# Kernel tuning notes

Measured on AMD Instinct MI355X. Metric: run time of the kernel, lower is better.

## Reference

```python
import jax, jax.numpy as jnp
import numpy as np

N_NODES = 100000


def gcn_conv(x, W, b, src, dst, n_nodes):
    """PyG-style GCNConv: add self-loops, symmetric D^-1/2 (A+I) D^-1/2 normalization,
    linear transform, scatter-add aggregation, bias."""
    h = x @ W  # [N, out]
    # add self-loops
    loop = jnp.arange(n_nodes, dtype=src.dtype)
    src_all = jnp.concatenate([src, loop])
    dst_all = jnp.concatenate([dst, loop])
    # degree (of A + I) counted at destination nodes
    deg = jax.ops.segment_sum(jnp.ones_like(dst_all, dtype=h.dtype), dst_all,
                              num_segments=n_nodes)
    dinv = jnp.where(deg > 0, jax.lax.rsqrt(deg), 0.0)  # [N]
    w = dinv[src_all] * dinv[dst_all]                   # per-edge norm
    msg = h[src_all] * w[:, None]                       # gather + scale
    out = jax.ops.segment_sum(msg, dst_all, num_segments=n_nodes)
    return out + b


def setup_inputs() -> dict:
    key = jax.random.key(0)
    k1, k2, k3, k4 = jax.random.split(key, 4)
    n, e = N_NODES, 1600000
    d_in, d_hid, d_out = 128, 128, 64
    x = jax.random.normal(k1, (n, d_in), dtype=jnp.float32)
    edge_index = jax.random.randint(k2, (2, e), 0, n, dtype=jnp.int64)
    W1 = jax.random.normal(k3, (d_in, d_hid), dtype=jnp.float32) / np.sqrt(d_in)
    b1 = jnp.zeros((d_hid,), dtype=jnp.float32)
    W2 = jax.random.normal(k4, (d_hid, d_out), dtype=jnp.float32) / np.sqrt(d_hid)
    b2 = jnp.zeros((d_out,), dtype=jnp.float32)
    return {"x": x, "edge_index": edge_index, "W1": W1, "b1": b1, "W2": W2, "b2": b2}


def reference(x, edge_index, W1, b1, W2, b2):
    src, dst = edge_index[0], edge_index[1]
    h = jax.nn.relu(gcn_conv(x, W1, b1, src, dst, N_NODES))
    return gcn_conv(h, W2, b2, src, dst, N_NODES)
```

## Files before the change

kernel.cpp:

```cpp
#include <hip/hip_runtime.h>
#include <hip/hip_fp16.h>


typedef _Float16 half8 __attribute__((ext_vector_type(8)));
typedef float f32x4 __attribute__((ext_vector_type(4)));

constexpr int BK_SHIFT = 7;
constexpr int BK_NODES = 1 << BK_SHIFT;
constexpr int NB_MAX   = 1024;
constexpr int SLAB     = 2560;
constexpr int P1_EPT   = 32;
constexpr int P1_EDGES = 256 * P1_EPT;

__global__ __launch_bounds__(256) void k_p1(const int* __restrict__ src,
                                            const int* __restrict__ dst, int E,
                                            int NB, int* __restrict__ bfill,
                                            unsigned* __restrict__ slab) {
  __shared__ unsigned stage[P1_EDGES];
  __shared__ unsigned short bidp[P1_EDGES];
  __shared__ int hist[NB_MAX];
  __shared__ int lbase[NB_MAX];
  __shared__ int goff[NB_MAX];
  __shared__ int part[256];

  const int t = threadIdx.x;
  const long base = (long)blockIdx.x * P1_EDGES;
  const int nval = (int)(((long)E - base < (long)P1_EDGES) ? (E - base) : P1_EDGES);

  for (int i = t; i < NB; i += 256) hist[i] = 0;
  __syncthreads();

  int eb[P1_EPT];
  unsigned ev[P1_EPT];
#pragma unroll
  for (int i = 0; i < P1_EPT; ++i) {
    long e = base + t + i * 256;
    int b = -1;
    unsigned v = 0;
    if (e < E) {
      int d = dst[e];
      int s = src[e];
      b = d >> BK_SHIFT;
      v = ((unsigned)(d & (BK_NODES - 1)) << 17) | (unsigned)s;
      atomicAdd(&hist[b], 1);
    }
    eb[i] = b;
    ev[i] = v;
  }
  __syncthreads();

  int lc[4];
  int lsum = 0;
#pragma unroll
  for (int j = 0; j < 4; ++j) {
    int b = t * 4 + j;
    lc[j] = (b < NB) ? hist[b] : 0;
    lsum += lc[j];
  }
  part[t] = lsum;
  __syncthreads();
  for (int o = 1; o < 256; o <<= 1) {
    int a = (t >= o) ? part[t - o] : 0;
    __syncthreads();
    part[t] += a;
    __syncthreads();
  }
  int run = part[t] - lsum;
#pragma unroll
  for (int j = 0; j < 4; ++j) {
    int b = t * 4 + j;
    if (b < NB) lbase[b] = run;
    run += lc[j];
  }
  __syncthreads();

  for (int b = t; b < NB; b += 256) {
    int len = hist[b];
    int g = len ? atomicAdd(&bfill[b], len) : 0;
    goff[b] = b * SLAB + g - lbase[b];
  }
  __syncthreads();

#pragma unroll
  for (int i = 0; i < P1_EPT; ++i) {
    if (eb[i] >= 0) {
      int p = atomicAdd(&lbase[eb[i]], 1);
      stage[p] = ev[i];
      bidp[p] = (unsigned short)eb[i];
    }
  }
  __syncthreads();

  for (int p = t; p < nval; p += 256) {
    int b = bidp[p];
    slab[goff[b] + p] = stage[p];
  }
}

__global__ __launch_bounds__(1024) void k_bscan(const int* __restrict__ bfill, int NB,
                                                int* __restrict__ bbase) {
  __shared__ int sm[1024];
  const int t = threadIdx.x;
  int v = (t < NB) ? bfill[t] : 0;
  sm[t] = v;
  __syncthreads();
  for (int o = 1; o < 1024; o <<= 1) {
    int a = (t >= o) ? sm[t - o] : 0;
    __syncthreads();
    sm[t] += a;
    __syncthreads();
  }
  if (t < NB) bbase[t] = sm[t] - v;
}

__global__ __launch_bounds__(256) void k_p2(const unsigned* __restrict__ slab,
                                            const int* __restrict__ bfill,
                                            const int* __restrict__ bbase, int N,
                                            int* __restrict__ deg,
                                            int* __restrict__ row_ptr,
                                            float* __restrict__ dinv,
                                            int* __restrict__ ssrc) {
  __shared__ int hist[BK_NODES];
  __shared__ int lb[BK_NODES];
  const int b = blockIdx.x;
  const int t = threadIdx.x;
  const int len = bfill[b];
  const int gbase = bbase[b];
  const unsigned* seg = slab + (size_t)b * SLAB;

  if (t < BK_NODES) hist[t] = 0;
  __syncthreads();
  for (int i = t; i < len; i += 256) atomicAdd(&hist[seg[i] >> 17], 1);
  __syncthreads();

  if (t < BK_NODES) lb[t] = hist[t];
  __syncthreads();
  for (int o = 1; o < BK_NODES; o <<= 1) {
    int a = 0;
    if (t < BK_NODES && t >= o) a = lb[t - o];
    __syncthreads();
    if (t < BK_NODES) lb[t] += a;
    __syncthreads();
  }

  int n = b * BK_NODES + t;
  if (t < BK_NODES && n < N) {
    int d = hist[t];
    deg[n] = d;
    row_ptr[n] = gbase + lb[t] - d;
    dinv[n] = rsqrtf((float)(d + 1));
  }
  __syncthreads();
  if (t < BK_NODES) lb[t] -= hist[t];
  __syncthreads();

  for (int i = t; i < len; i += 256) {
    unsigned v = seg[i];
    int l = v >> 17;
    int p = atomicAdd(&lb[l], 1);
    ssrc[gbase + p] = (int)(v & 0x1FFFF);
  }
}

__global__ __launch_bounds__(256) void k_prep(const float* __restrict__ W1,
                                              const float* __restrict__ W2,
                                              __half* __restrict__ Wt1,
                                              __half* __restrict__ Wt2) {
  int i = blockIdx.x * blockDim.x + threadIdx.x;
  if (i < 16384) {
    int k = i >> 7, n = i & 127;
    Wt1[n * 128 + k] = __float2half(W1[i]);
  } else if (i < 24576) {
    int j = i - 16384;
    int k = j >> 6, n = j & 63;
    Wt2[n * 128 + k] = __float2half(W2[j]);
  }
}

template <int NC, bool IN_HALF>
__global__ __launch_bounds__(256) void k_gemm(const void* __restrict__ Xv,
                                              const __half* __restrict__ Wt,
                                              const float* __restrict__ dinv,
                                              __half* __restrict__ H, int N) {
  constexpr int K = 128;
  constexpr int BM = 64;
  constexpr int LDK = K + 8;
  constexpr int NT = NC / 16;
  __shared__ _Float16 xs[BM * LDK];
  __shared__ _Float16 wl[NC * LDK];

  const int t = threadIdx.x;
  const int r0 = blockIdx.x * BM;

  if (IN_HALF) {
    const __half* X = (const __half*)Xv;
    for (int i = t; i < BM * (K / 8); i += 256) {
      int row = i >> 4, kc = i & 15;
      float4 raw = make_float4(0.f, 0.f, 0.f, 0.f);
      if (r0 + row < N)
        raw = *reinterpret_cast<const float4*>(X + (size_t)(r0 + row) * K + 8 * kc);
      *reinterpret_cast<float4*>(&xs[row * LDK + 8 * kc]) = raw;
    }
  } else {
    const float* X = (const float*)Xv;
    for (int i = t; i < BM * (K / 4); i += 256) {
      int row = i >> 5, kg = i & 31;
      float4 v = make_float4(0.f, 0.f, 0.f, 0.f);
      if (r0 + row < N)
        v = *reinterpret_cast<const float4*>(X + (size_t)(r0 + row) * K + 4 * kg);
      union { _Float16 h[4]; unsigned long long u; } pk;
      pk.h[0] = (_Float16)v.x; pk.h[1] = (_Float16)v.y;
      pk.h[2] = (_Float16)v.z; pk.h[3] = (_Float16)v.w;
      *reinterpret_cast<unsigned long long*>(&xs[row * LDK + 4 * kg]) = pk.u;
    }
  }
  for (int i = t; i < NC * (K / 8); i += 256) {
    int n = i >> 4, kc = i & 15;
    float4 raw = *reinterpret_cast<const float4*>(Wt + (size_t)n * K + 8 * kc);
    *reinterpret_cast<float4*>(&wl[n * LDK + 8 * kc]) = raw;
  }
  __syncthreads();

  const int w = t >> 6;
  const int lane = t & 63;
  const int lm = lane & 15;
  const int lg = lane >> 4;

  half8 a[4];
#pragma unroll
  for (int kt = 0; kt < 4; ++kt)
    a[kt] = *reinterpret_cast<const half8*>(&xs[(w * 16 + lm) * LDK + kt * 32 + lg * 8]);

  f32x4 acc[NT];
#pragma unroll
  for (int nt = 0; nt < NT; ++nt) acc[nt] = (f32x4){0.f, 0.f, 0.f, 0.f};

#pragma unroll
  for (int nt = 0; nt < NT; ++nt) {
#pragma unroll
    for (int kt = 0; kt < 4; ++kt) {
      half8 b = *reinterpret_cast<const half8*>(
          &wl[(nt * 16 + lm) * LDK + kt * 32 + lg * 8]);
      acc[nt] = __builtin_amdgcn_mfma_f32_16x16x32_f16(a[kt], b, acc[nt], 0, 0, 0);
    }
  }

  float dv[4];
#pragma unroll
  for (int r = 0; r < 4; ++r) {
    int row = r0 + w * 16 + lg * 4 + r;
    dv[r] = (row < N) ? dinv[row] : 0.f;
  }
#pragma unroll
  for (int nt = 0; nt < NT; ++nt) {
#pragma unroll
    for (int r = 0; r < 4; ++r) {
      int row = r0 + w * 16 + lg * 4 + r;
      if (row < N)
        H[(size_t)row * NC + nt * 16 + lm] = __float2half(acc[nt][r] * dv[r]);
    }
  }
}

__global__ __launch_bounds__(256) void k_agg128(const __half* __restrict__ H,
                                                const int* __restrict__ rp,
                                                const int* __restrict__ dg,
                                                const int* __restrict__ ssrc,
                                                const float* __restrict__ dinv,
                                                const float* __restrict__ bias,
                                                __half* __restrict__ out, int N) {
  const int wave = threadIdx.x >> 6;
  const int lane = threadIdx.x & 63;
  const int n = blockIdx.x * 4 + wave;
  if (n >= N) return;

  const int eh = lane >> 4;
  const int cl = lane & 15;
  const int e0 = rp[n];
  const int e1 = e0 + dg[n];
  const float dv = dinv[n];

  float acc[8] = {0.f, 0.f, 0.f, 0.f, 0.f, 0.f, 0.f, 0.f};
  auto gat = [&](int s) {
    half8 v = *reinterpret_cast<const half8*>(H + (size_t)s * 128 + 8 * cl);
#pragma unroll
    for (int j = 0; j < 8; ++j) acc[j] += (float)v[j];
  };
  if (eh == 0) gat(n);
  int e = e0;
  for (; e + 8 <= e1; e += 8) {
    int sA = ssrc[e + eh];
    int sB = ssrc[e + 4 + eh];
    gat(sA);
    gat(sB);
  }
  if (e + 4 <= e1) { gat(ssrc[e + eh]); e += 4; }
  if (e + eh < e1) gat(ssrc[e + eh]);

#pragma unroll
  for (int j = 0; j < 8; ++j) {
    acc[j] += __shfl_xor(acc[j], 16);
    acc[j] += __shfl_xor(acc[j], 32);
  }
  if (eh == 0) {
    float4 b0 = *reinterpret_cast<const float4*>(bias + 8 * cl);
    float4 b1 = *reinterpret_cast<const float4*>(bias + 8 * cl + 4);
    float o[8];
    o[0] = acc[0] * dv + b0.x; o[1] = acc[1] * dv + b0.y;
    o[2] = acc[2] * dv + b0.z; o[3] = acc[3] * dv + b0.w;
    o[4] = acc[4] * dv + b1.x; o[5] = acc[5] * dv + b1.y;
    o[6] = acc[6] * dv + b1.z; o[7] = acc[7] * dv + b1.w;
    half8 ph;
#pragma unroll
    for (int j = 0; j < 8; ++j) ph[j] = (_Float16)fmaxf(o[j], 0.f);
    *reinterpret_cast<half8*>(out + (size_t)n * 128 + 8 * cl) = ph;
  }
}

__global__ __launch_bounds__(256) void k_agg64(const __half* __restrict__ H,
                                               const int* __restrict__ rp,
                                               const int* __restrict__ dg,
                                               const int* __restrict__ ssrc,
                                               const float* __restrict__ dinv,
                                               const float* __restrict__ bias,
                                               float* __restrict__ out, int N) {
  const int wave = threadIdx.x >> 6;
  const int lane = threadIdx.x & 63;
  const int n = blockIdx.x * 4 + wave;
  if (n >= N) return;

  const int eh = lane >> 3;
  const int cl = lane & 7;
  const int e0 = rp[n];
  const int e1 = e0 + dg[n];
  const float dv = dinv[n];

  float acc[8] = {0.f, 0.f, 0.f, 0.f, 0.f, 0.f, 0.f, 0.f};
  auto gat = [&](int s) {
    half8 v = *reinterpret_cast<const half8*>(H + (size_t)s * 64 + 8 * cl);
#pragma unroll
    for (int j = 0; j < 8; ++j) acc[j] += (float)v[j];
  };
  if (eh == 0) gat(n);
  int e = e0;
  for (; e + 16 <= e1; e += 16) {
    int sA = ssrc[e + eh];
    int sB = ssrc[e + 8 + eh];
    gat(sA);
    gat(sB);
  }
  if (e + 8 <= e1) { gat(ssrc[e + eh]); e += 8; }
  if (e + eh < e1) gat(ssrc[e + eh]);

#pragma unroll
  for (int j = 0; j < 8; ++j) {
    acc[j] += __shfl_xor(acc[j], 8);
    acc[j] += __shfl_xor(acc[j], 16);
    acc[j] += __shfl_xor(acc[j], 32);
  }
  if (eh == 0) {
    float4 b0 = *reinterpret_cast<const float4*>(bias + 8 * cl);
    float4 b1 = *reinterpret_cast<const float4*>(bias + 8 * cl + 4);
    f32x4 o0, o1;
    o0[0] = acc[0] * dv + b0.x; o0[1] = acc[1] * dv + b0.y;
    o0[2] = acc[2] * dv + b0.z; o0[3] = acc[3] * dv + b0.w;
    o1[0] = acc[4] * dv + b1.x; o1[1] = acc[5] * dv + b1.y;
    o1[2] = acc[6] * dv + b1.z; o1[3] = acc[7] * dv + b1.w;
    float* op = out + (size_t)n * 64 + 8 * cl;
    __builtin_nontemporal_store(o0, reinterpret_cast<f32x4*>(op));
    __builtin_nontemporal_store(o1, reinterpret_cast<f32x4*>(op + 4));
  }
}

extern "C" void kernel_launch(void* const* d_in, const int* in_sizes, int n_in,
                              void* d_out, int out_size, void* d_ws, size_t ws_size,
                              hipStream_t stream) {
  const float* x = (const float*)d_in[0];
  const int* ei = (const int*)d_in[1];
  const float* W1 = (const float*)d_in[2];
  const float* b1 = (const float*)d_in[3];
  const float* W2 = (const float*)d_in[4];
  const float* b2 = (const float*)d_in[5];

  const int K = 128;
  const int N = in_sizes[0] / K;
  const int E = in_sizes[1] / 2;
  const int NB = (N + BK_NODES - 1) >> BK_SHIFT;
  if (NB > NB_MAX) return;

  const int* src = ei;
  const int* dst = ei + E;

  size_t off = 0;
  auto carve = [&](size_t bytes) {
    size_t o = off;
    off += (bytes + 255) & ~(size_t)255;
    return o;
  };
  char* ws = (char*)d_ws;
  int*      deg     = (int*)(ws + carve((size_t)N * 4));
  int*      row_ptr = (int*)(ws + carve((size_t)N * 4));
  float*    dinv    = (float*)(ws + carve((size_t)N * 4));
  int*      bfill   = (int*)(ws + carve((size_t)NB * 4));
  int*      bbase   = (int*)(ws + carve((size_t)NB * 4));
  __half*   wt1     = (__half*)(ws + carve(16384 * 2));
  __half*   wt2     = (__half*)(ws + carve(8192 * 2));
  unsigned* slab    = (unsigned*)(ws + carve((size_t)NB * SLAB * 4));
  int*      ssrc    = (int*)(ws + carve((size_t)E * 4));
  __half*   h1      = (__half*)(ws + carve((size_t)N * K * 2));
  __half*   out1    = (__half*)(ws + carve((size_t)N * K * 2));
  if (off > ws_size) return;

  __half* h2 = h1;
  float* out2 = (float*)d_out;

  (void)hipMemsetAsync(bfill, 0, (size_t)NB * 4, stream);
  k_prep<<<96, 256, 0, stream>>>(W1, W2, wt1, wt2);
  const int nwg1 = (E + P1_EDGES - 1) / P1_EDGES;
  k_p1<<<nwg1, 256, 0, stream>>>(src, dst, E, NB, bfill, slab);
  k_bscan<<<1, 1024, 0, stream>>>(bfill, NB, bbase);
  k_p2<<<NB, 256, 0, stream>>>(slab, bfill, bbase, N, deg, row_ptr, dinv, ssrc);

  k_gemm<128, false><<<(N + 63) / 64, 256, 0, stream>>>(x, wt1, dinv, h1, N);
  k_agg128<<<(N + 3) / 4, 256, 0, stream>>>(h1, row_ptr, deg, ssrc, dinv, b1,
                                            out1, N);
  k_gemm<64, true><<<(N + 63) / 64, 256, 0, stream>>>(out1, wt2, dinv, h2, N);
  k_agg64<<<(N + 3) / 4, 256, 0, stream>>>(h2, row_ptr, deg, ssrc, dinv, b2,
                                           out2, N);
  (void)n_in; (void)out_size;
}
```

Measured before the change: 201.1 us.

## Split layer-1 features into two 64-column slabs for cache-friendly aggregation

The first GEMM now writes its fp16 output as two contiguous column slabs of 64 features each, instead of interleaved 128-wide rows. The layer-1 aggregation launches twice as many blocks, one per slice, and each wave gathers 128-byte rows from a single slab with 8 edges in flight per step. The aim is to halve the working set each gather pass touches, so the random neighbor reads hit L2/MALL more often. The cost is reading the index stream and running the edge loop twice.

```diff
diff --git a/kernel.cpp b/kernel.cpp
--- a/kernel.cpp
+++ b/kernel.cpp
@@ -177,7 +177,7 @@
   }
 }
 
-template <int NC, bool IN_HALF>
+template <int NC, bool IN_HALF, bool OUT_SLAB>
 __global__ __launch_bounds__(256) void k_gemm(const void* __restrict__ Xv,
                                               const __half* __restrict__ Wt,
                                               const float* __restrict__ dinv,
@@ -256,55 +256,68 @@
 #pragma unroll
     for (int r = 0; r < 4; ++r) {
       int row = r0 + w * 16 + lg * 4 + r;
-      if (row < N)
-        H[(size_t)row * NC + nt * 16 + lm] = __float2half(acc[nt][r] * dv[r]);
-    }
-  }
-}
-
-__global__ __launch_bounds__(256) void k_agg128(const __half* __restrict__ H,
-                                                const int* __restrict__ rp,
-                                                const int* __restrict__ dg,
-                                                const int* __restrict__ ssrc,
-                                                const float* __restrict__ dinv,
-                                                const float* __restrict__ bias,
-                                                __half* __restrict__ out, int N) {
+      if (row < N) {
+        _Float16 val = (_Float16)(acc[nt][r] * dv[r]);
+        if (OUT_SLAB) {
+          int sl = nt >> 2;
+          int cc = (nt & 3) * 16 + lm;
+          *(_Float16*)(H + (size_t)sl * N * 64 + (size_t)row * 64 + cc) = val;
+        } else {
+          *(_Float16*)(H + (size_t)row * NC + nt * 16 + lm) = val;
+        }
+      }
+    }
+  }
+}
+
+__global__ __launch_bounds__(256) void k_agg128s(const __half* __restrict__ Hs,
+                                                 const int* __restrict__ rp,
+                                                 const int* __restrict__ dg,
+                                                 const int* __restrict__ ssrc,
+                                                 const float* __restrict__ dinv,
+                                                 const float* __restrict__ bias,
+                                                 __half* __restrict__ out, int N) {
+  const int slice = blockIdx.x & 1;
+  const int g = blockIdx.x >> 1;
   const int wave = threadIdx.x >> 6;
   const int lane = threadIdx.x & 63;
-  const int n = blockIdx.x * 4 + wave;
+  const int n = g * 4 + wave;
   if (n >= N) return;
 
-  const int eh = lane >> 4;
-  const int cl = lane & 15;
+  const int eh = lane >> 3;
+  const int cl = lane & 7;
+  const __half* __restrict__ sp = Hs + (size_t)slice * N * 64;
   const int e0 = rp[n];
   const int e1 = e0 + dg[n];
   const float dv = dinv[n];
 
   float acc[8] = {0.f, 0.f, 0.f, 0.f, 0.f, 0.f, 0.f, 0.f};
   auto gat = [&](int s) {
-    half8 v = *reinterpret_cast<const half8*>(H + (size_t)s * 128 + 8 * cl);
+    half8 v = *reinterpret_cast<const half8*>(sp + (size_t)s * 64 + 8 * cl);
 #pragma unroll
     for (int j = 0; j < 8; ++j) acc[j] += (float)v[j];
   };
   if (eh == 0) gat(n);
   int e = e0;
-  for (; e + 8 <= e1; e += 8) {
+  for (; e + 16 <= e1; e += 16) {
     int sA = ssrc[e + eh];
-    int sB = ssrc[e + 4 + eh];
+    int sB = ssrc[e + 8 + eh];
     gat(sA);
     gat(sB);
   }
-  if (e + 4 <= e1) { gat(ssrc[e + eh]); e += 4; }
+  if (e + 8 <= e1) { gat(ssrc[e + eh]); e += 8; }
   if (e + eh < e1) gat(ssrc[e + eh]);
 
 #pragma unroll
   for (int j = 0; j < 8; ++j) {
+    acc[j] += __shfl_xor(acc[j], 8);
     acc[j] += __shfl_xor(acc[j], 16);
     acc[j] += __shfl_xor(acc[j], 32);
   }
   if (eh == 0) {
-    float4 b0 = *reinterpret_cast<const float4*>(bias + 8 * cl);
-    float4 b1 = *reinterpret_cast<const float4*>(bias + 8 * cl + 4);
+    const float* bp = bias + slice * 64 + 8 * cl;
+    float4 b0 = *reinterpret_cast<const float4*>(bp);
+    float4 b1 = *reinterpret_cast<const float4*>(bp + 4);
     float o[8];
     o[0] = acc[0] * dv + b0.x; o[1] = acc[1] * dv + b0.y;
     o[2] = acc[2] * dv + b0.z; o[3] = acc[3] * dv + b0.w;
@@ -313,7 +326,7 @@
     half8 ph;
 #pragma unroll
     for (int j = 0; j < 8; ++j) ph[j] = (_Float16)fmaxf(o[j], 0.f);
-    *reinterpret_cast<half8*>(out + (size_t)n * 128 + 8 * cl) = ph;
+    *reinterpret_cast<half8*>(out + (size_t)n * 128 + slice * 64 + 8 * cl) = ph;
   }
 }
 
@@ -421,10 +434,10 @@
   k_bscan<<<1, 1024, 0, stream>>>(bfill, NB, bbase);
   k_p2<<<NB, 256, 0, stream>>>(slab, bfill, bbase, N, deg, row_ptr, dinv, ssrc);
 
-  k_gemm<128, false><<<(N + 63) / 64, 256, 0, stream>>>(x, wt1, dinv, h1, N);
-  k_agg128<<<(N + 3) / 4, 256, 0, stream>>>(h1, row_ptr, deg, ssrc, dinv, b1,
-                                            out1, N);
-  k_gemm<64, true><<<(N + 63) / 64, 256, 0, stream>>>(out1, wt2, dinv, h2, N);
+  k_gemm<128, false, true><<<(N + 63) / 64, 256, 0, stream>>>(x, wt1, dinv, h1, N);
+  k_agg128s<<<((N + 3) / 4) * 2, 256, 0, stream>>>(h1, row_ptr, deg, ssrc, dinv,
+                                                   b1, out1, N);
+  k_gemm<64, true, false><<<(N + 63) / 64, 256, 0, stream>>>(out1, wt2, dinv, h2, N);
   k_agg64<<<(N + 3) / 4, 256, 0, stream>>>(h2, row_ptr, deg, ssrc, dinv, b2,
                                            out2, N);
   (void)n_in; (void)out_size;
```

Result: slower. 218.6 us (+8.7%).
